# Performance work log

Hardware: AMD Instinct MI355X
Metric: run time of the kernel (lower is better)

Reference implementation:

```python
import jax, jax.numpy as jnp
import numpy as np
from jax import lax

P = 32   # patch_size
D = 128  # emb_dim
E = 8    # num_experts
K = 2    # top-k
C = 3    # in_channels


def _conv(x, w, b, stride, groups, pad):
    y = lax.conv_general_dilated(
        x, w, (stride, stride), [(pad, pad), (pad, pad)],
        feature_group_count=groups,
        dimension_numbers=('NCHW', 'OIHW', 'NCHW'))
    return jax.nn.relu(y + b[None, :, None, None])


def setup_inputs() -> dict:
    key = jax.random.key(0)
    ks = jax.random.split(key, 16)
    s = 0.02
    inp = {
        'x': jax.random.normal(ks[0], (16, C, 512, 512), dtype=jnp.float32),
        'gate_w1': jax.random.normal(ks[1], (C * P * P, D), dtype=jnp.float32) * s,
        'gate_b1': jnp.zeros((D,), jnp.float32),
        'gate_w2': jax.random.normal(ks[2], (D, E), dtype=jnp.float32) * s,
        'gate_b2': jnp.zeros((E,), jnp.float32),
        'dw1_w': jax.random.normal(ks[3], (E, C, 1, 3, 3), dtype=jnp.float32) * s,
        'dw1_b': jnp.zeros((E, C), jnp.float32),
        'pw1_w': jax.random.normal(ks[4], (E, D, C, 1, 1), dtype=jnp.float32) * s,
        'pw1_b': jnp.zeros((E, D), jnp.float32),
        'dw2_w': jax.random.normal(ks[5], (E, D, 1, 3, 3), dtype=jnp.float32) * s,
        'dw2_b': jnp.zeros((E, D), jnp.float32),
        'pw2_w': jax.random.normal(ks[6], (E, D, D, 1, 1), dtype=jnp.float32) * s,
        'pw2_b': jnp.zeros((E, D), jnp.float32),
    }
    return inp


def reference(x, gate_w1, gate_b1, gate_w2, gate_b2,
              dw1_w, dw1_b, pw1_w, pw1_b, dw2_w, dw2_b, pw2_w, pw2_b):
    B, Cc, H, W = x.shape
    hp, wp = H // P, W // P
    N = hp * wp
    BN = B * N
    # nn.Unfold(kernel=stride=P) -> non-overlapping patches, (c,i,j) flatten order
    patches = x.reshape(B, Cc, hp, P, wp, P)
    patches = patches.transpose(0, 2, 4, 1, 3, 5).reshape(B, N, Cc * P * P)
    # gate MLP
    h = jax.nn.relu(patches @ gate_w1 + gate_b1)
    logits = h @ gate_w2 + gate_b2              # [B,N,E]
    topk_vals, topk_idx = lax.top_k(logits, K)  # sorted descending, like torch
    weights = jax.nn.softmax(topk_vals, axis=-1)
    patches_sp = patches.reshape(BN, Cc, P, P)
    # dense per-expert depthwise-separable conv stacks (small fixed loop over E)
    outs = []
    for e in range(E):
        y = _conv(patches_sp, dw1_w[e], dw1_b[e], 2, Cc, 1)  # [BN,C,16,16]
        y = _conv(y, pw1_w[e], pw1_b[e], 1, 1, 0)            # [BN,D,16,16]
        y = _conv(y, dw2_w[e], dw2_b[e], 2, D, 1)            # [BN,D,8,8]
        y = _conv(y, pw2_w[e], pw2_b[e], 1, 1, 0)            # [BN,D,8,8]
        outs.append(y.mean(axis=(2, 3)))                     # adaptive avg pool 1
    expert_outs = jnp.stack(outs, axis=1)                    # [BN,E,D]
    idx = topk_idx.reshape(BN, K)
    w = weights.reshape(BN, K)
    sel = jnp.take_along_axis(expert_outs, idx[:, :, None], axis=1)  # [BN,K,D]
    out = (w[:, :, None] * sel).sum(axis=1)                  # [BN,D]
    return out.reshape(B, hp, wp, D).transpose(0, 3, 1, 2)
```

## Files before the change

### kernel.cpp

```cpp
#include <hip/hip_runtime.h>

#define NPATCH 4096
#define NFRAG 49152

typedef __attribute__((ext_vector_type(8))) __bf16 bf16x8;
typedef __attribute__((ext_vector_type(4))) __bf16 bf16x4;
typedef __attribute__((ext_vector_type(4))) float f32x4;

__global__ __launch_bounds__(256) void prep_kernel(const float* __restrict__ pw2_w,
                                                   bf16x8* __restrict__ wpk) {
  int tid = blockIdx.x * 256 + threadIdx.x;
  int l = tid & 63, nt = (tid >> 6) & 7, kt = (tid >> 9) & 3, e = tid >> 11;
  int n = nt * 16 + (l & 15);
  int k = kt * 32 + (l >> 4) * 8;
  const float* src = &pw2_w[((size_t)(e * 128 + n)) * 128 + k];
  float4 a = *(const float4*)src;
  float4 b = *(const float4*)(src + 4);
  bf16x8 r = { (__bf16)a.x, (__bf16)a.y, (__bf16)a.z, (__bf16)a.w,
               (__bf16)b.x, (__bf16)b.y, (__bf16)b.z, (__bf16)b.w };
  wpk[tid] = r;
}

__global__ __launch_bounds__(256) void prep_w1(const float* __restrict__ w1,
                                               bf16x8* __restrict__ w1f) {
  int tid = blockIdx.x * 256 + threadIdx.x;
  int l = tid & 63, nt = (tid >> 6) & 7, ktg = tid >> 9;
  int k0 = ktg * 32 + (l >> 4) * 8, d = nt * 16 + (l & 15);
  bf16x8 h, lo;
#pragma unroll
  for (int j = 0; j < 8; ++j) {
    float v = w1[(size_t)(k0 + j) * 128 + d];
    __bf16 hv = (__bf16)v;
    h[j] = hv;
    lo[j] = (__bf16)(v - (float)hv);
  }
  w1f[tid] = h;
  w1f[NFRAG + tid] = lo;
}

#define GATE_DECLS                                                                  \
  const int t  = threadIdx.x;                                                       \
  const int l  = t & 63;                                                            \
  const int wv = t >> 6;                                                            \
  const int mrow  = l & 15;                                                         \
  const int kslot = l >> 4;                                                         \
  const int sp   = l & 15;                                                          \
  const int sj4  = (l >> 4) + 4 * (wv & 1);                                         \
  const int srr0 = (wv >> 1);                                                       \
  const int srr1 = 4 + (wv >> 1);

#define SLOAD(ch, R0, R1) do {                                                      \
    R0 = *(const float4*)&x[pbase + (size_t)((ch) >> 2) * 262144 +                  \
                            (size_t)(((ch) & 3) * 8 + srr0) * 512 + sj4 * 4];       \
    R1 = *(const float4*)&x[pbase + (size_t)((ch) >> 2) * 262144 +                  \
                            (size_t)(((ch) & 3) * 8 + srr1) * 512 + sj4 * 4];       \
  } while (0)

#define SPLIT4(V, HP, LP) do {                                                      \
    bf16x4 h_, lo_;                                                                 \
    h_[0] = (__bf16)V.x; lo_[0] = (__bf16)(V.x - (float)h_[0]);                     \
    h_[1] = (__bf16)V.y; lo_[1] = (__bf16)(V.y - (float)h_[1]);                     \
    h_[2] = (__bf16)V.z; lo_[2] = (__bf16)(V.z - (float)h_[2]);                     \
    h_[3] = (__bf16)V.w; lo_[3] = (__bf16)(V.w - (float)h_[3]);                     \
    *(bf16x4*)(HP) = h_; *(bf16x4*)(LP) = lo_;                                      \
  } while (0)

#define SSTORE(ch, R0, R1) do {                                                     \
    const int bf_ = (ch) & 1;                                                       \
    SPLIT4(R0, &Ah[bf_][srr0][(sj4 >> 1) * 16 + sp][(sj4 & 1) * 4],                 \
               &Al[bf_][srr0][(sj4 >> 1) * 16 + sp][(sj4 & 1) * 4]);                \
    SPLIT4(R1, &Ah[bf_][srr1][(sj4 >> 1) * 16 + sp][(sj4 & 1) * 4],                 \
               &Al[bf_][srr1][(sj4 >> 1) * 16 + sp][(sj4 & 1) * 4]);                \
  } while (0)

#define BLOAD(ch, BH, BL) do {                                                      \
    const bf16x8* wp_ = w1f + (size_t)(ch) * 4096 + wv * 64 + l;                    \
    _Pragma("unroll")                                                               \
    for (int q = 0; q < 8; ++q) { BH[q] = wp_[q * 512]; BL[q] = wp_[NFRAG + q * 512]; } \
  } while (0)

#define MFMA_PASS(ch, BH, BL) do {                                                  \
    const int bf_ = (ch) & 1;                                                       \
    _Pragma("unroll")                                                               \
    for (int ktl = 0; ktl < 8; ++ktl) {                                             \
      bf16x8 ah_ = *(const bf16x8*)&Ah[bf_][ktl][l][0];                             \
      bf16x8 al_ = *(const bf16x8*)&Al[bf_][ktl][l][0];                             \
      const int r_ = ktl & 3;                                                       \
      accA[r_] = __builtin_amdgcn_mfma_f32_16x16x32_bf16(ah_, BH[ktl], accA[r_], 0, 0, 0); \
      accB[r_] = __builtin_amdgcn_mfma_f32_16x16x32_bf16(ah_, BL[ktl], accB[r_], 0, 0, 0); \
      accB[r_] = __builtin_amdgcn_mfma_f32_16x16x32_bf16(al_, BH[ktl], accB[r_], 0, 0, 0); \
    }                                                                               \
  } while (0)

__global__ __launch_bounds__(512) void gate_mfma_split(
    const float* __restrict__ x, const bf16x8* __restrict__ w1f,
    float* __restrict__ hpart)
{
  __shared__ __bf16 Ah[2][8][64][8];
  __shared__ __bf16 Al[2][8][64][8];

  GATE_DECLS
  const int kh = blockIdx.x & 1;
  const int p0 = (blockIdx.x >> 1) * 16;
  const int cb = kh * 6;

  size_t pbase;
  {
    int gp = p0 + sp;
    int bb = gp >> 8, ph = (gp >> 4) & 15, pwc = gp & 15;
    pbase = ((size_t)(bb * 3) * 512 + ph * 32) * 512 + pwc * 32;
  }

  f32x4 accA[4], accB[4];
#pragma unroll
  for (int i = 0; i < 4; ++i) {
    accA[i] = (f32x4){0.f, 0.f, 0.f, 0.f};
    accB[i] = (f32x4){0.f, 0.f, 0.f, 0.f};
  }

  float4 r0, r1;
  bf16x8 bh0[8], bl0[8], bh1[8], bl1[8];

  SLOAD(cb + 0, r0, r1);
  BLOAD(cb + 0, bh0, bl0);
  SSTORE(cb + 0, r0, r1);
  __syncthreads();

#pragma unroll
  for (int cc = 0; cc < 6; cc += 2) {
    if (cc + 1 < 6) { SLOAD(cb + cc + 1, r0, r1); BLOAD(cb + cc + 1, bh1, bl1); }
    MFMA_PASS(cb + cc, bh0, bl0);
    if (cc + 1 < 6) SSTORE(cb + cc + 1, r0, r1);
    __syncthreads();
    if (cc + 2 < 6) { SLOAD(cb + cc + 2, r0, r1); BLOAD(cb + cc + 2, bh0, bl0); }
    MFMA_PASS(cb + cc + 1, bh1, bl1);
    if (cc + 2 < 6) SSTORE(cb + cc + 2, r0, r1);
    __syncthreads();
  }

  {
    f32x4 sA = (accA[0] + accA[1]) + (accA[2] + accA[3]);
    f32x4 sB = (accB[0] + accB[1]) + (accB[2] + accB[3]);
    const int d = wv * 16 + mrow;
#pragma unroll
    for (int r = 0; r < 4; ++r) {
      int m = kslot * 4 + r;
      hpart[((size_t)kh * NPATCH + p0 + m) * 128 + d] = sA[r] + sB[r];
    }
  }
}

__global__ __launch_bounds__(256) void gate_logits(
    const float* __restrict__ hpart, const float* __restrict__ b1,
    const float* __restrict__ w2, const float* __restrict__ b2,
    int* __restrict__ gidx, float* __restrict__ gw)
{
  __shared__ float hs[16][128];
  __shared__ float ls[16][8];
  const int t  = threadIdx.x;
  const int p0 = blockIdx.x * 16;

  for (int i = t; i < 2048; i += 256) {
    int p = i >> 7, d = i & 127;
    float h0 = hpart[((size_t)(p0 + p)) * 128 + d];
    float h1 = hpart[((size_t)NPATCH + p0 + p) * 128 + d];
    hs[p][d] = fmaxf((h0 + h1) + b1[d], 0.f);
  }
  __syncthreads();

  if (t < 128) {
    int p = t >> 3, e = t & 7;
    float s = 0.f;
    for (int d0 = 0; d0 < 128; d0 += 32) {
      float cs = 0.f;
#pragma unroll
      for (int dd = 0; dd < 32; ++dd)
        cs = fmaf(hs[p][d0 + dd], w2[(d0 + dd) * 8 + e], cs);
      s += cs;
    }
    ls[p][e] = s + b2[e];
  }
  __syncthreads();

  if (t < 16) {
    int gp = p0 + t;
    float v[8];
#pragma unroll
    for (int e = 0; e < 8; ++e) v[e] = ls[t][e];
    int e0 = 0;
#pragma unroll
    for (int e = 1; e < 8; ++e) if (v[e] > v[e0]) e0 = e;
    int e1 = (e0 == 0) ? 1 : 0;
#pragma unroll
    for (int e = 0; e < 8; ++e) { if (e != e0 && v[e] > v[e1]) e1 = e; }
    float bexp = expf(v[e1] - v[e0]);
    float inv  = 1.f / (1.f + bexp);
    gidx[gp * 2 + 0] = e0;
    gidx[gp * 2 + 1] = e1;
    gw[gp * 2 + 0] = inv;
    gw[gp * 2 + 1] = bexp * inv;
  }
}

__global__ __launch_bounds__(512) void gate_mfma(
    const float* __restrict__ x, const bf16x8* __restrict__ w1f,
    const float* __restrict__ b1, const float* __restrict__ w2,
    const float* __restrict__ b2, int* __restrict__ gidx,
    float* __restrict__ gw)
{
  __shared__ __bf16 Ah[2][8][64][8];
  __shared__ __bf16 Al[2][8][64][8];
  __shared__ float hs[16][128];
  __shared__ float ls[16][8];

  GATE_DECLS
  const int p0 = blockIdx.x * 16;

  size_t pbase;
  {
    int gp = p0 + sp;
    int bb = gp >> 8, ph = (gp >> 4) & 15, pwc = gp & 15;
    pbase = ((size_t)(bb * 3) * 512 + ph * 32) * 512 + pwc * 32;
  }

  f32x4 accA[4], accB[4];
#pragma unroll
  for (int i = 0; i < 4; ++i) {
    accA[i] = (f32x4){0.f, 0.f, 0.f, 0.f};
    accB[i] = (f32x4){0.f, 0.f, 0.f, 0.f};
  }

  float4 r0, r1;
  bf16x8 bh0[8], bl0[8], bh1[8], bl1[8];

  SLOAD(0, r0, r1);
  BLOAD(0, bh0, bl0);
  SSTORE(0, r0, r1);
  __syncthreads();

#pragma unroll
  for (int cc = 0; cc < 12; cc += 2) {
    if (cc + 1 < 12) { SLOAD(cc + 1, r0, r1); BLOAD(cc + 1, bh1, bl1); }
    MFMA_PASS(cc, bh0, bl0);
    if (cc + 1 < 12) SSTORE(cc + 1, r0, r1);
    __syncthreads();
    if (cc + 2 < 12) { SLOAD(cc + 2, r0, r1); BLOAD(cc + 2, bh0, bl0); }
    MFMA_PASS(cc + 1, bh1, bl1);
    if (cc + 2 < 12) SSTORE(cc + 2, r0, r1);
    __syncthreads();
  }

  {
    f32x4 sA = (accA[0] + accA[1]) + (accA[2] + accA[3]);
    f32x4 sB = (accB[0] + accB[1]) + (accB[2] + accB[3]);
    const int d = wv * 16 + mrow;
    const float bb1 = b1[d];
#pragma unroll
    for (int r = 0; r < 4; ++r) {
      int m = kslot * 4 + r;
      hs[m][d] = fmaxf(sA[r] + sB[r] + bb1, 0.f);
    }
  }
  __syncthreads();

  if (t < 128) {
    int p = t >> 3, e = t & 7;
    float s = 0.f;
    for (int d0 = 0; d0 < 128; d0 += 32) {
      float cs = 0.f;
#pragma unroll
      for (int dd = 0; dd < 32; ++dd)
        cs = fmaf(hs[p][d0 + dd], w2[(d0 + dd) * 8 + e], cs);
      s += cs;
    }
    ls[p][e] = s + b2[e];
  }
  __syncthreads();

  if (t < 16) {
    int gp = p0 + t;
    float v[8];
#pragma unroll
    for (int e = 0; e < 8; ++e) v[e] = ls[t][e];
    int e0 = 0;
#pragma unroll
    for (int e = 1; e < 8; ++e) if (v[e] > v[e0]) e0 = e;
    int e1 = (e0 == 0) ? 1 : 0;
#pragma unroll
    for (int e = 0; e < 8; ++e) { if (e != e0 && v[e] > v[e1]) e1 = e; }
    float bexp = expf(v[e1] - v[e0]);
    float inv  = 1.f / (1.f + bexp);
    gidx[gp * 2 + 0] = e0;
    gidx[gp * 2 + 1] = e1;
    gw[gp * 2 + 0] = inv;
    gw[gp * 2 + 1] = bexp * inv;
  }
}

__global__ __launch_bounds__(512, 4) void gate_kernel(
    const float* __restrict__ x, const float* __restrict__ w1,
    const float* __restrict__ b1, const float* __restrict__ w2,
    const float* __restrict__ b2, int* __restrict__ gidx,
    float* __restrict__ gw)
{
  __shared__ float As[8][1024];
  __shared__ float hs[8][128];
  __shared__ float ls[8][8];

  const int t   = threadIdx.x;
  const int p0  = blockIdx.x * 8;
  const int d   = t & 127;
  const int grp = t >> 7;
  const int pa  = grp * 2, pb = grp * 2 + 1;

  float acc0 = 0.f, acc1 = 0.f;

  for (int c = 0; c < 3; ++c) {
#pragma unroll
    for (int it = 0; it < 4; ++it) {
      int i = t + it * 512;
      int p = i >> 8, rem = i & 255, r = rem >> 3, j4 = (rem & 7) * 4;
      int gp = p0 + p;
      int bb = gp >> 8, ph = (gp >> 4) & 15, pwc = gp & 15;
      *(float4*)&As[p][r * 32 + j4] =
          *(const float4*)&x[((size_t)(bb * 3 + c) * 512 + ph * 32 + r) * 512 + pwc * 32 + j4];
    }
    __syncthreads();

    const float* wdp = w1 + (size_t)c * 131072 + d;
    for (int ch = 0; ch < 32; ++ch) {
      float bv[32];
#pragma unroll
      for (int j = 0; j < 32; ++j) bv[j] = wdp[(ch * 32 + j) * 128];
      const int kl = ch * 32;
      float ca = 0.f, cb = 0.f;
#pragma unroll
      for (int q = 0; q < 8; ++q) {
        float4 a0 = *(const float4*)&As[pa][kl + q * 4];
        float4 a1 = *(const float4*)&As[pb][kl + q * 4];
        ca = fmaf(a0.x, bv[q * 4 + 0], ca); ca = fmaf(a0.y, bv[q * 4 + 1], ca);
        ca = fmaf(a0.z, bv[q * 4 + 2], ca); ca = fmaf(a0.w, bv[q * 4 + 3], ca);
        cb = fmaf(a1.x, bv[q * 4 + 0], cb); cb = fmaf(a1.y, bv[q * 4 + 1], cb);
        cb = fmaf(a1.z, bv[q * 4 + 2], cb); cb = fmaf(a1.w, bv[q * 4 + 3], cb);
      }
      acc0 += ca; acc1 += cb;
    }
    __syncthreads();
  }

  hs[pa][d] = fmaxf(acc0 + b1[d], 0.f);
  hs[pb][d] = fmaxf(acc1 + b1[d], 0.f);
  __syncthreads();

  if (t < 64) {
    int p = t >> 3, e = t & 7;
    float s = 0.f;
    for (int d0 = 0; d0 < 128; d0 += 32) {
      float cs = 0.f;
#pragma unroll
      for (int dd = 0; dd < 32; ++dd)
        cs = fmaf(hs[p][d0 + dd], w2[(d0 + dd) * 8 + e], cs);
      s += cs;
    }
    ls[p][e] = s + b2[e];
  }
  __syncthreads();

  if (t < 8) {
    int gp = p0 + t;
    float v[8];
#pragma unroll
    for (int e = 0; e < 8; ++e) v[e] = ls[t][e];
    int e0 = 0;
#pragma unroll
    for (int e = 1; e < 8; ++e) if (v[e] > v[e0]) e0 = e;
    int e1 = (e0 == 0) ? 1 : 0;
#pragma unroll
    for (int e = 0; e < 8; ++e) { if (e != e0 && v[e] > v[e1]) e1 = e; }
    float bexp = expf(v[e1] - v[e0]);
    float inv  = 1.f / (1.f + bexp);
    gidx[gp * 2 + 0] = e0;
    gidx[gp * 2 + 1] = e1;
    gw[gp * 2 + 0] = inv;
    gw[gp * 2 + 1] = bexp * inv;
  }
}

#define EXPERT_COMMON_PRE                                                          \
  __shared__ float  ps[3][32][36];                                                 \
  __shared__ float  y1s[3][256];                                                   \
  __shared__ __bf16 y3b[64][140];                                                  \
  __shared__ float  posum[4][128];                                                 \
  __shared__ float  outbuf[128];                                                   \
  const int t  = threadIdx.x;                                                      \
  const int gp = blockIdx.x;                                                       \
  const int b = gp >> 8, ph = (gp >> 4) & 15, pw = gp & 15;                        \
  const int l = t & 63, wv = t >> 6;                                               \
  _Pragma("unroll")                                                                \
  for (int it = 0; it < 3; ++it) {                                                 \
    int f4i = t + 256 * it;                                                        \
    int c = f4i >> 8, r = (f4i >> 3) & 31, j4 = f4i & 7;                           \
    *(float4*)&ps[c][r][j4 * 4] =                                                  \
        *(const float4*)&x[((size_t)(b * 3 + c) * 512 + ph * 32 + r) * 512 +       \
                           pw * 32 + j4 * 4];                                      \
  }                                                                                \
  if (t < 128) outbuf[t] = 0.f;                                                    \
  const int dd   = t & 127;                                                        \
  const int half = t >> 7;                                                         \
  __syncthreads();

#define EXPERT_PHASES_1_2                                                          \
    for (int oi = t; oi < 768; oi += 256) {                                        \
      int c = oi >> 8, p = (oi >> 4) & 15, q = oi & 15;                            \
      float a = dw1_b[e * 3 + c];                                                  \
      const float* wp_ = &dw1_w[(e * 3 + c) * 9];                                  \
      _Pragma("unroll")                                                            \
      for (int di = 0; di < 3; ++di) {                                             \
        int ii = 2 * p + di - 1;                                                   \
        if (ii < 0) continue;                                                      \
        _Pragma("unroll")                                                          \
        for (int dj = 0; dj < 3; ++dj) {                                           \
          int jj = 2 * q + dj - 1;                                                 \
          if (jj < 0) continue;                                                    \
          a = fmaf(wp_[di * 3 + dj], ps[c][ii][jj], a);                            \
        }                                                                          \
      }                                                                            \
      y1s[c][p * 16 + q] = fmaxf(a, 0.f);                                          \
    }                                                                              \
    __syncthreads();                                                               \
    {                                                                              \
      const float pwa = pw1_w[(e * 128 + dd) * 3 + 0];                             \
      const float pwb = pw1_w[(e * 128 + dd) * 3 + 1];                             \
      const float pwc = pw1_w[(e * 128 + dd) * 3 + 2];                             \
      const float pb  = pw1_b[e * 128 + dd];                                       \
      float dwv[9];                                                                \
      _Pragma("unroll")                                                            \
      for (int i = 0; i < 9; ++i) dwv[i] = dw2_w[(e * 128 + dd) * 9 + i];          \
      const float db = dw2_b[e * 128 + dd];                                        \
      for (int u = half * 4; u < half * 4 + 4; ++u) {                              \
        float vacc[8];                                                             \
        _Pragma("unroll")                                                          \
        for (int v = 0; v < 8; ++v) vacc[v] = db;                                  \
        _Pragma("unroll")                                                          \
        for (int di = 0; di < 3; ++di) {                                           \
          int ii = 2 * u + di - 1;                                                 \
          if (ii < 0) continue;                                                    \
          float y2row[16];                                                         \
          _Pragma("unroll")                                                        \
          for (int q4 = 0; q4 < 4; ++q4) {                                         \
            float4 a  = *(const float4*)&y1s[0][ii * 16 + q4 * 4];                 \
            float4 bq = *(const float4*)&y1s[1][ii * 16 + q4 * 4];                 \
            float4 cq = *(const float4*)&y1s[2][ii * 16 + q4 * 4];                 \
            y2row[q4 * 4 + 0] = fmaxf(fmaf(pwa, a.x, fmaf(pwb, bq.x, fmaf(pwc, cq.x, pb))), 0.f); \
            y2row[q4 * 4 + 1] = fmaxf(fmaf(pwa, a.y, fmaf(pwb, bq.y, fmaf(pwc, cq.y, pb))), 0.f); \
            y2row[q4 * 4 + 2] = fmaxf(fmaf(pwa, a.z, fmaf(pwb, bq.z, fmaf(pwc, cq.z, pb))), 0.f); \
            y2row[q4 * 4 + 3] = fmaxf(fmaf(pwa, a.w, fmaf(pwb, bq.w, fmaf(pwc, cq.w, pb))), 0.f); \
          }                                                                        \
          _Pragma("unroll")                                                        \
          for (int v = 0; v < 8; ++v) {                                            \
            _Pragma("unroll")                                                      \
            for (int dj = 0; dj < 3; ++dj) {                                       \
              int jj = 2 * v + dj - 1;                                             \
              if (jj < 0) continue;                                                \
              vacc[v] = fmaf(dwv[di * 3 + dj], y2row[jj], vacc[v]);                \
            }                                                                      \
          }                                                                        \
        }                                                                          \
        _Pragma("unroll")                                                          \
        for (int v = 0; v < 8; ++v)                                                \
          y3b[u * 8 + v][dd] = (__bf16)fmaxf(vacc[v], 0.f);                        \
      }                                                                            \
    }

#define EXPERT_EPILOG                                                              \
    _Pragma("unroll")                                                              \
    for (int nt = 0; nt < 8; ++nt) {                                               \
      float bias = pw2_b[e * 128 + nt * 16 + (l & 15)];                            \
      float s = fmaxf(acc[nt][0] + bias, 0.f) + fmaxf(acc[nt][1] + bias, 0.f)      \
              + fmaxf(acc[nt][2] + bias, 0.f) + fmaxf(acc[nt][3] + bias, 0.f);     \
      s += __shfl_xor(s, 16);                                                      \
      s += __shfl_xor(s, 32);                                                      \
      if (l < 16) posum[wv][nt * 16 + l] = s;                                      \
    }

__global__ __launch_bounds__(256, 4) void expert_packed(
    const float* __restrict__ x,
    const float* __restrict__ dw1_w, const float* __restrict__ dw1_b,
    const float* __restrict__ pw1_w, const float* __restrict__ pw1_b,
    const float* __restrict__ dw2_w, const float* __restrict__ dw2_b,
    const bf16x8* __restrict__ wpk, const float* __restrict__ pw2_b,
    const int* __restrict__ gidx, const float* __restrict__ gw,
    float* __restrict__ out)
{
  EXPERT_COMMON_PRE
  for (int k = 0; k < 2; ++k) {
    const int   e  = gidx[gp * 2 + k];
    const float wk = gw[gp * 2 + k];
    EXPERT_PHASES_1_2
    __syncthreads();
    {
      f32x4 acc[8];
#pragma unroll
      for (int nt = 0; nt < 8; ++nt) acc[nt] = (f32x4){0.f, 0.f, 0.f, 0.f};
      const int row  = wv * 16 + (l & 15);
      const int kofs = (l >> 4) * 8;
      bf16x8 afrag[4];
#pragma unroll
      for (int kt = 0; kt < 4; ++kt)
        afrag[kt] = *(const bf16x8*)&y3b[row][kt * 32 + kofs];
      const bf16x8* wb = wpk + (size_t)e * 2048 + l;
#pragma unroll
      for (int kt = 0; kt < 4; ++kt) {
        bf16x8 bf[8];
#pragma unroll
        for (int nt = 0; nt < 8; ++nt) bf[nt] = wb[(kt * 8 + nt) * 64];
#pragma unroll
        for (int nt = 0; nt < 8; ++nt)
          acc[nt] = __builtin_amdgcn_mfma_f32_16x16x32_bf16(afrag[kt], bf[nt], acc[nt], 0, 0, 0);
      }
      EXPERT_EPILOG
    }
    __syncthreads();
    if (t < 128)
      outbuf[t] += wk * 0.015625f *
                   (posum[0][t] + posum[1][t] + posum[2][t] + posum[3][t]);
    __syncthreads();
  }
  if (t < 128)
    out[((size_t)(b * 128 + t) * 16 + ph) * 16 + pw] = outbuf[t];
}

__global__ __launch_bounds__(256) void expert_fb(
    const float* __restrict__ x,
    const float* __restrict__ dw1_w, const float* __restrict__ dw1_b,
    const float* __restrict__ pw1_w, const float* __restrict__ pw1_b,
    const float* __restrict__ dw2_w, const float* __restrict__ dw2_b,
    const float* __restrict__ pw2_w, const float* __restrict__ pw2_b,
    const int* __restrict__ gidx, const float* __restrict__ gw,
    float* __restrict__ out)
{
  __shared__ __bf16 wlds[128][136];
  EXPERT_COMMON_PRE
  for (int k = 0; k < 2; ++k) {
    const int   e  = gidx[gp * 2 + k];
    const float wk = gw[gp * 2 + k];
    EXPERT_PHASES_1_2
    for (int i4 = t; i4 < 4096; i4 += 256) {
      int n = i4 >> 5, kq = i4 & 31;
      float4 w4 = *(const float4*)&pw2_w[((size_t)(e * 128 + n)) * 128 + kq * 4];
      bf16x4 pk = { (__bf16)w4.x, (__bf16)w4.y, (__bf16)w4.z, (__bf16)w4.w };
      *(bf16x4*)&wlds[n][kq * 4] = pk;
    }
    __syncthreads();
    {
      f32x4 acc[8];
#pragma unroll
      for (int nt = 0; nt < 8; ++nt) acc[nt] = (f32x4){0.f, 0.f, 0.f, 0.f};
      const int row  = wv * 16 + (l & 15);
      const int kofs = (l >> 4) * 8;
      bf16x8 afrag[4];
#pragma unroll
      for (int kt = 0; kt < 4; ++kt)
        afrag[kt] = *(const bf16x8*)&y3b[row][kt * 32 + kofs];
#pragma unroll
      for (int kt = 0; kt < 4; ++kt) {
#pragma unroll
        for (int nt = 0; nt < 8; ++nt) {
          bf16x8 bfrag = *(const bf16x8*)&wlds[nt * 16 + (l & 15)][kt * 32 + kofs];
          acc[nt] = __builtin_amdgcn_mfma_f32_16x16x32_bf16(afrag[kt], bfrag, acc[nt], 0, 0, 0);
        }
      }
      EXPERT_EPILOG
    }
    __syncthreads();
    if (t < 128)
      outbuf[t] += wk * 0.015625f *
                   (posum[0][t] + posum[1][t] + posum[2][t] + posum[3][t]);
    __syncthreads();
  }
  if (t < 128)
    out[((size_t)(b * 128 + t) * 16 + ph) * 16 + pw] = outbuf[t];
}

extern "C" void kernel_launch(void* const* d_in, const int* in_sizes, int n_in,
                              void* d_out, int out_size, void* d_ws, size_t ws_size,
                              hipStream_t stream) {
  const float* x       = (const float*)d_in[0];
  const float* gate_w1 = (const float*)d_in[1];
  const float* gate_b1 = (const float*)d_in[2];
  const float* gate_w2 = (const float*)d_in[3];
  const float* gate_b2 = (const float*)d_in[4];
  const float* dw1_w   = (const float*)d_in[5];
  const float* dw1_b   = (const float*)d_in[6];
  const float* pw1_w   = (const float*)d_in[7];
  const float* pw1_b   = (const float*)d_in[8];
  const float* dw2_w   = (const float*)d_in[9];
  const float* dw2_b   = (const float*)d_in[10];
  const float* pw2_w   = (const float*)d_in[11];
  const float* pw2_b   = (const float*)d_in[12];
  float* out = (float*)d_out;

  const size_t off_wpk   = (size_t)NPATCH * 4 * sizeof(int);
  const size_t off_w1f   = off_wpk + 256 * 1024;
  const size_t off_hpart = off_w1f + (size_t)NFRAG * 2 * 16;
  const size_t ws_pack   = off_w1f;
  const size_t ws_full   = off_hpart;
  const size_t ws_split  = off_hpart + (size_t)2 * NPATCH * 128 * sizeof(float);

  int*    gidx  = (int*)d_ws;
  float*  gw    = (float*)((char*)d_ws + (size_t)NPATCH * 2 * sizeof(int));
  bf16x8* wpk   = (bf16x8*)((char*)d_ws + off_wpk);
  bf16x8* w1f   = (bf16x8*)((char*)d_ws + off_w1f);
  float*  hpart = (float*)((char*)d_ws + off_hpart);

  const bool packed  = ws_size >= ws_pack;
  const bool mfgate  = ws_size >= ws_full;
  const bool splitk  = ws_size >= ws_split;

  if (splitk) {
    prep_w1<<<192, 256, 0, stream>>>(gate_w1, w1f);
    gate_mfma_split<<<512, 512, 0, stream>>>(x, w1f, hpart);
    gate_logits<<<NPATCH / 16, 256, 0, stream>>>(hpart, gate_b1, gate_w2, gate_b2, gidx, gw);
  } else if (mfgate) {
    prep_w1<<<192, 256, 0, stream>>>(gate_w1, w1f);
    gate_mfma<<<NPATCH / 16, 512, 0, stream>>>(x, w1f, gate_b1, gate_w2, gate_b2, gidx, gw);
  } else {
    gate_kernel<<<NPATCH / 8, 512, 0, stream>>>(x, gate_w1, gate_b1, gate_w2, gate_b2, gidx, gw);
  }
  if (packed) {
    prep_kernel<<<64, 256, 0, stream>>>(pw2_w, wpk);
    expert_packed<<<NPATCH, 256, 0, stream>>>(x, dw1_w, dw1_b, pw1_w, pw1_b,
                                              dw2_w, dw2_b, wpk, pw2_b, gidx, gw, out);
  } else {
    expert_fb<<<NPATCH, 256, 0, stream>>>(x, dw1_w, dw1_b, pw1_w, pw1_b,
                                          dw2_w, dw2_b, pw2_w, pw2_b, gidx, gw, out);
  }
}
```

Measured before the change: 246.5 us.

## Pre-pack input patches into bf16 MFMA fragments and run gate GEMM per wave

Adds a prep_x kernel that converts the input patches into split hi/lo bf16 fragments laid out for MFMA. A new single-wave-per-block gate_wave kernel then computes one 16x16 output tile over the full K, with no shared memory or block barriers, writing the full hidden activations. This replaces the split-K shared-memory gate GEMM and removes the partial-sum reduction. The cost is an extra pass that writes about 50MB of packed fragments and reads them back, plus extra workspace.

```diff
diff --git a/kernel.cpp b/kernel.cpp
--- a/kernel.cpp
+++ b/kernel.cpp
@@ -2,6 +2,7 @@
 
 #define NPATCH 4096
 #define NFRAG 49152
+#define NA    1572864
 
 typedef __attribute__((ext_vector_type(8))) __bf16 bf16x8;
 typedef __attribute__((ext_vector_type(4))) __bf16 bf16x4;
@@ -38,6 +39,119 @@
   w1f[NFRAG + tid] = lo;
 }
 
+__global__ __launch_bounds__(256) void prep_x(const float* __restrict__ x,
+                                              bf16x8* __restrict__ afr) {
+  int tid = blockIdx.x * 256 + threadIdx.x;
+  int l   = tid & 63;
+  int mt  = (tid >> 6) & 255;
+  int ktg = tid >> 14;
+  int gp = mt * 16 + (l & 15);
+  int b = gp >> 8, ph = (gp >> 4) & 15, pwc = gp & 15;
+  int k0 = ktg * 32 + (l >> 4) * 8;
+  int c = k0 >> 10, r = (k0 >> 5) & 31, j = k0 & 31;
+  const float* src = &x[((size_t)(b * 3 + c) * 512 + ph * 32 + r) * 512 + pwc * 32 + j];
+  float4 v0 = *(const float4*)src;
+  float4 v1 = *(const float4*)(src + 4);
+  float av[8] = {v0.x, v0.y, v0.z, v0.w, v1.x, v1.y, v1.z, v1.w};
+  bf16x8 h, lo;
+#pragma unroll
+  for (int q = 0; q < 8; ++q) {
+    __bf16 hv = (__bf16)av[q];
+    h[q] = hv;
+    lo[q] = (__bf16)(av[q] - (float)hv);
+  }
+  afr[tid] = h;
+  afr[NA + tid] = lo;
+}
+
+__global__ __launch_bounds__(64) void gate_wave(
+    const bf16x8* __restrict__ afr, const bf16x8* __restrict__ w1f,
+    float* __restrict__ hfull)
+{
+  const int l  = threadIdx.x;
+  const int mt = blockIdx.x & 255;
+  const int nt = blockIdx.x >> 8;
+  const bf16x8* Ap = afr + (size_t)mt * 64 + l;
+  const bf16x8* Bp = w1f + (size_t)nt * 64 + l;
+
+  f32x4 accA[4], accB[4];
+#pragma unroll
+  for (int i = 0; i < 4; ++i) {
+    accA[i] = (f32x4){0.f, 0.f, 0.f, 0.f};
+    accB[i] = (f32x4){0.f, 0.f, 0.f, 0.f};
+  }
+
+#pragma unroll 4
+  for (int kt = 0; kt < 96; ++kt) {
+    bf16x8 ah = Ap[(size_t)kt * 16384];
+    bf16x8 al = Ap[(size_t)kt * 16384 + NA];
+    bf16x8 bh = Bp[(size_t)kt * 512];
+    bf16x8 bl = Bp[(size_t)kt * 512 + NFRAG];
+    const int r_ = kt & 3;
+    accA[r_] = __builtin_amdgcn_mfma_f32_16x16x32_bf16(ah, bh, accA[r_], 0, 0, 0);
+    accB[r_] = __builtin_amdgcn_mfma_f32_16x16x32_bf16(ah, bl, accB[r_], 0, 0, 0);
+    accB[r_] = __builtin_amdgcn_mfma_f32_16x16x32_bf16(al, bh, accB[r_], 0, 0, 0);
+  }
+
+  f32x4 sA = (accA[0] + accA[1]) + (accA[2] + accA[3]);
+  f32x4 sB = (accB[0] + accB[1]) + (accB[2] + accB[3]);
+  const int d  = nt * 16 + (l & 15);
+  const int m0 = mt * 16 + (l >> 4) * 4;
+#pragma unroll
+  for (int r = 0; r < 4; ++r)
+    hfull[(size_t)(m0 + r) * 128 + d] = sA[r] + sB[r];
+}
+
+__global__ __launch_bounds__(256) void gate_logits(
+    const float* __restrict__ hfull, const float* __restrict__ b1,
+    const float* __restrict__ w2, const float* __restrict__ b2,
+    int* __restrict__ gidx, float* __restrict__ gw)
+{
+  __shared__ float hs[16][128];
+  __shared__ float ls[16][8];
+  const int t  = threadIdx.x;
+  const int p0 = blockIdx.x * 16;
+
+  for (int i = t; i < 2048; i += 256) {
+    int p = i >> 7, d = i & 127;
+    hs[p][d] = fmaxf(hfull[((size_t)(p0 + p)) * 128 + d] + b1[d], 0.f);
+  }
+  __syncthreads();
+
+  if (t < 128) {
+    int p = t >> 3, e = t & 7;
+    float s = 0.f;
+    for (int d0 = 0; d0 < 128; d0 += 32) {
+      float cs = 0.f;
+#pragma unroll
+      for (int dd = 0; dd < 32; ++dd)
+        cs = fmaf(hs[p][d0 + dd], w2[(d0 + dd) * 8 + e], cs);
+      s += cs;
+    }
+    ls[p][e] = s + b2[e];
+  }
+  __syncthreads();
+
+  if (t < 16) {
+    int gp = p0 + t;
+    float v[8];
+#pragma unroll
+    for (int e = 0; e < 8; ++e) v[e] = ls[t][e];
+    int e0 = 0;
+#pragma unroll
+    for (int e = 1; e < 8; ++e) if (v[e] > v[e0]) e0 = e;
+    int e1 = (e0 == 0) ? 1 : 0;
+#pragma unroll
+    for (int e = 0; e < 8; ++e) { if (e != e0 && v[e] > v[e1]) e1 = e; }
+    float bexp = expf(v[e1] - v[e0]);
+    float inv  = 1.f / (1.f + bexp);
+    gidx[gp * 2 + 0] = e0;
+    gidx[gp * 2 + 1] = e1;
+    gw[gp * 2 + 0] = inv;
+    gw[gp * 2 + 1] = bexp * inv;
+  }
+}
+
 #define GATE_DECLS                                                                  \
   const int t  = threadIdx.x;                                                       \
   const int l  = t & 63;                                                            \
@@ -91,116 +205,6 @@
       accB[r_] = __builtin_amdgcn_mfma_f32_16x16x32_bf16(al_, BH[ktl], accB[r_], 0, 0, 0); \
     }                                                                               \
   } while (0)
-
-__global__ __launch_bounds__(512) void gate_mfma_split(
-    const float* __restrict__ x, const bf16x8* __restrict__ w1f,
-    float* __restrict__ hpart)
-{
-  __shared__ __bf16 Ah[2][8][64][8];
-  __shared__ __bf16 Al[2][8][64][8];
-
-  GATE_DECLS
-  const int kh = blockIdx.x & 1;
-  const int p0 = (blockIdx.x >> 1) * 16;
-  const int cb = kh * 6;
-
-  size_t pbase;
-  {
-    int gp = p0 + sp;
-    int bb = gp >> 8, ph = (gp >> 4) & 15, pwc = gp & 15;
-    pbase = ((size_t)(bb * 3) * 512 + ph * 32) * 512 + pwc * 32;
-  }
-
-  f32x4 accA[4], accB[4];
-#pragma unroll
-  for (int i = 0; i < 4; ++i) {
-    accA[i] = (f32x4){0.f, 0.f, 0.f, 0.f};
-    accB[i] = (f32x4){0.f, 0.f, 0.f, 0.f};
-  }
-
-  float4 r0, r1;
-  bf16x8 bh0[8], bl0[8], bh1[8], bl1[8];
-
-  SLOAD(cb + 0, r0, r1);
-  BLOAD(cb + 0, bh0, bl0);
-  SSTORE(cb + 0, r0, r1);
-  __syncthreads();
-
-#pragma unroll
-  for (int cc = 0; cc < 6; cc += 2) {
-    if (cc + 1 < 6) { SLOAD(cb + cc + 1, r0, r1); BLOAD(cb + cc + 1, bh1, bl1); }
-    MFMA_PASS(cb + cc, bh0, bl0);
-    if (cc + 1 < 6) SSTORE(cb + cc + 1, r0, r1);
-    __syncthreads();
-    if (cc + 2 < 6) { SLOAD(cb + cc + 2, r0, r1); BLOAD(cb + cc + 2, bh0, bl0); }
-    MFMA_PASS(cb + cc + 1, bh1, bl1);
-    if (cc + 2 < 6) SSTORE(cb + cc + 2, r0, r1);
-    __syncthreads();
-  }
-
-  {
-    f32x4 sA = (accA[0] + accA[1]) + (accA[2] + accA[3]);
-    f32x4 sB = (accB[0] + accB[1]) + (accB[2] + accB[3]);
-    const int d = wv * 16 + mrow;
-#pragma unroll
-    for (int r = 0; r < 4; ++r) {
-      int m = kslot * 4 + r;
-      hpart[((size_t)kh * NPATCH + p0 + m) * 128 + d] = sA[r] + sB[r];
-    }
-  }
-}
-
-__global__ __launch_bounds__(256) void gate_logits(
-    const float* __restrict__ hpart, const float* __restrict__ b1,
-    const float* __restrict__ w2, const float* __restrict__ b2,
-    int* __restrict__ gidx, float* __restrict__ gw)
-{
-  __shared__ float hs[16][128];
-  __shared__ float ls[16][8];
-  const int t  = threadIdx.x;
-  const int p0 = blockIdx.x * 16;
-
-  for (int i = t; i < 2048; i += 256) {
-    int p = i >> 7, d = i & 127;
-    float h0 = hpart[((size_t)(p0 + p)) * 128 + d];
-    float h1 = hpart[((size_t)NPATCH + p0 + p) * 128 + d];
-    hs[p][d] = fmaxf((h0 + h1) + b1[d], 0.f);
-  }
-  __syncthreads();
-
-  if (t < 128) {
-    int p = t >> 3, e = t & 7;
-    float s = 0.f;
-    for (int d0 = 0; d0 < 128; d0 += 32) {
-      float cs = 0.f;
-#pragma unroll
-      for (int dd = 0; dd < 32; ++dd)
-        cs = fmaf(hs[p][d0 + dd], w2[(d0 + dd) * 8 + e], cs);
-      s += cs;
-    }
-    ls[p][e] = s + b2[e];
-  }
-  __syncthreads();
-
-  if (t < 16) {
-    int gp = p0 + t;
-    float v[8];
-#pragma unroll
-    for (int e = 0; e < 8; ++e) v[e] = ls[t][e];
-    int e0 = 0;
-#pragma unroll
-    for (int e = 1; e < 8; ++e) if (v[e] > v[e0]) e0 = e;
-    int e1 = (e0 == 0) ? 1 : 0;
-#pragma unroll
-    for (int e = 0; e < 8; ++e) { if (e != e0 && v[e] > v[e1]) e1 = e; }
-    float bexp = expf(v[e1] - v[e0]);
-    float inv  = 1.f / (1.f + bexp);
-    gidx[gp * 2 + 0] = e0;
-    gidx[gp * 2 + 1] = e1;
-    gw[gp * 2 + 0] = inv;
-    gw[gp * 2 + 1] = bexp * inv;
-  }
-}
 
 __global__ __launch_bounds__(512) void gate_mfma(
     const float* __restrict__ x, const bf16x8* __restrict__ w1f,
@@ -602,25 +606,28 @@
 
   const size_t off_wpk   = (size_t)NPATCH * 4 * sizeof(int);
   const size_t off_w1f   = off_wpk + 256 * 1024;
-  const size_t off_hpart = off_w1f + (size_t)NFRAG * 2 * 16;
+  const size_t off_afr   = off_w1f + (size_t)NFRAG * 2 * 16;
+  const size_t off_hfull = off_afr + (size_t)NA * 2 * 16;
   const size_t ws_pack   = off_w1f;
-  const size_t ws_full   = off_hpart;
-  const size_t ws_split  = off_hpart + (size_t)2 * NPATCH * 128 * sizeof(float);
+  const size_t ws_full   = off_afr;
+  const size_t ws_wavegt = off_hfull + (size_t)NPATCH * 128 * sizeof(float);
 
   int*    gidx  = (int*)d_ws;
   float*  gw    = (float*)((char*)d_ws + (size_t)NPATCH * 2 * sizeof(int));
   bf16x8* wpk   = (bf16x8*)((char*)d_ws + off_wpk);
   bf16x8* w1f   = (bf16x8*)((char*)d_ws + off_w1f);
-  float*  hpart = (float*)((char*)d_ws + off_hpart);
-
-  const bool packed  = ws_size >= ws_pack;
-  const bool mfgate  = ws_size >= ws_full;
-  const bool splitk  = ws_size >= ws_split;
-
-  if (splitk) {
+  bf16x8* afr   = (bf16x8*)((char*)d_ws + off_afr);
+  float*  hfull = (float*)((char*)d_ws + off_hfull);
+
+  const bool packed = ws_size >= ws_pack;
+  const bool mfgate = ws_size >= ws_full;
+  const bool wavegt = ws_size >= ws_wavegt;
+
+  if (wavegt) {
     prep_w1<<<192, 256, 0, stream>>>(gate_w1, w1f);
-    gate_mfma_split<<<512, 512, 0, stream>>>(x, w1f, hpart);
-    gate_logits<<<NPATCH / 16, 256, 0, stream>>>(hpart, gate_b1, gate_w2, gate_b2, gidx, gw);
+    prep_x<<<6144, 256, 0, stream>>>(x, afr);
+    gate_wave<<<2048, 64, 0, stream>>>(afr, w1f, hfull);
+    gate_logits<<<NPATCH / 16, 256, 0, stream>>>(hfull, gate_b1, gate_w2, gate_b2, gidx, gw);
   } else if (mfgate) {
     prep_w1<<<192, 256, 0, stream>>>(gate_w1, w1f);
     gate_mfma<<<NPATCH / 16, 512, 0, stream>>>(x, w1f, gate_b1, gate_w2, gate_b2, gidx, gw);
```

New measurement: 277.3 us. 1.12x slower.
